# Kernel tuning notes

Measured on AMD Instinct MI355X. Metric: run time of the kernel, lower is better.

The kernel has to match this reference:

```python
import jax, jax.numpy as jnp
import numpy as np

B, T = 2, 2048
D, H = 1024, 16
HD = D // H  # 64
L = 4
V = 32000
DFF = 4 * D
STD = 0.02


def layernorm(x, w, b, eps=1e-5):
    m = jnp.mean(x, axis=-1, keepdims=True)
    v = jnp.var(x, axis=-1, keepdims=True)
    return (x - m) / jnp.sqrt(v + eps) * w + b


def rope(x, cos, sin):
    # x: [B,H,T,HD]; cos/sin: [T, HD//2]
    xe = x[..., ::2]
    xo = x[..., 1::2]
    c = cos[None, None]
    s = sin[None, None]
    re = xe * c - xo * s
    ro = xe * s + xo * c
    return jnp.stack([re, ro], axis=-1).reshape(x.shape)


def setup_inputs() -> dict:
    key = jax.random.key(0)
    ks = jax.random.split(key, 16)
    n = lambda k, shp: jax.random.normal(k, shp, dtype=jnp.float32) * STD
    return {
        "idx": jax.random.randint(ks[0], (B, T), 0, V),
        "tok_emb": n(ks[1], (V, D)),
        "ln1_w": jnp.ones((L, D), jnp.float32),
        "ln1_b": jnp.zeros((L, D), jnp.float32),
        "Wq": n(ks[2], (L, D, D)),
        "Wk": n(ks[3], (L, D, D)),
        "Wv": n(ks[4], (L, D, D)),
        "Wp": n(ks[5], (L, D, D)),
        "ln2_w": jnp.ones((L, D), jnp.float32),
        "ln2_b": jnp.zeros((L, D), jnp.float32),
        "W1": n(ks[6], (L, D, DFF)),
        "b1": jnp.zeros((L, DFF), jnp.float32),
        "W2": n(ks[7], (L, DFF, D)),
        "b2": jnp.zeros((L, D), jnp.float32),
        "lnf_w": jnp.ones((D,), jnp.float32),
        "lnf_b": jnp.zeros((D,), jnp.float32),
    }


def reference(idx, tok_emb, ln1_w, ln1_b, Wq, Wk, Wv, Wp, ln2_w, ln2_b, W1, b1, W2, b2, lnf_w, lnf_b):
    x = tok_emb[idx]  # [B,T,D]
    # RoPE tables (base_freq=10000, no NTK since T == max_seq_len)
    freqs = 1.0 / (10000.0 ** (jnp.arange(0, HD, 2, dtype=jnp.float32) / HD))
    ang = jnp.arange(T, dtype=jnp.float32)[:, None] * freqs[None, :]  # [T, HD/2]
    cos, sin = jnp.cos(ang), jnp.sin(ang)
    causal = jnp.tril(jnp.ones((T, T), dtype=bool))

    def block(x, p):
        l1w, l1b, wq, wk, wv, wp, l2w, l2b, w1, bb1, w2, bb2 = p
        h = layernorm(x, l1w, l1b)
        q = (h @ wq).reshape(B, T, H, HD).transpose(0, 2, 1, 3)
        k = (h @ wk).reshape(B, T, H, HD).transpose(0, 2, 1, 3)
        v = (h @ wv).reshape(B, T, H, HD).transpose(0, 2, 1, 3)
        q = rope(q, cos, sin)
        k = rope(k, cos, sin)
        att = jnp.einsum('bhqd,bhkd->bhqk', q, k) / np.sqrt(HD).astype(np.float32)
        att = jnp.where(causal, att, -jnp.inf)
        att = jax.nn.softmax(att, axis=-1)
        y = jnp.einsum('bhqk,bhkd->bhqd', att, v)
        y = y.transpose(0, 2, 1, 3).reshape(B, T, D)
        x = x + y @ wp
        h2 = layernorm(x, l2w, l2b)
        # torch nn.GELU default = exact erf gelu
        x = x + (jax.nn.gelu(h2 @ w1 + bb1, approximate=False) @ w2 + bb2)
        return x, None

    params = (ln1_w, ln1_b, Wq, Wk, Wv, Wp, ln2_w, ln2_b, W1, b1, W2, b2)
    x, _ = jax.lax.scan(block, x, params)
    x = layernorm(x, lnf_w, lnf_b)
    logits = x @ tok_emb.T  # tied weights
    return logits
```

## Files before the change

kernel.cpp:

```cpp
#include <hip/hip_runtime.h>

#define Bv 2
#define Tv 2048
#define Dv 1024
#define Hv 16
#define HDv 64
#define Lv 4
#define Vv 32000
#define DFFv 4096
#define BTv (Bv * Tv)
#define D3v 3072

typedef __attribute__((ext_vector_type(8))) short bfrag_t;
typedef __attribute__((ext_vector_type(4))) float f4_t;

__device__ __forceinline__ unsigned short f2bf(float f) {
  union { float f; unsigned int u; } cv; cv.f = f;
  unsigned int u = cv.u;
  u += 0x7fffu + ((u >> 16) & 1u);
  return (unsigned short)(u >> 16);
}

__device__ __forceinline__ void gload16(const void* g, void* l) {
  __builtin_amdgcn_global_load_lds((__attribute__((address_space(1))) void*)g,
                                   (__attribute__((address_space(3))) void*)l, 16, 0, 0);
}

__global__ __launch_bounds__(256) void k_cvt(const float* __restrict__ src,
                                             unsigned short* __restrict__ dst, int n4) {
  int i = blockIdx.x * 256 + threadIdx.x;
  if (i >= n4) return;
  float4 v = ((const float4*)src)[i];
  ushort4 o;
  o.x = f2bf(v.x); o.y = f2bf(v.y); o.z = f2bf(v.z); o.w = f2bf(v.w);
  ((ushort4*)dst)[i] = o;
}

__global__ __launch_bounds__(256) void k_embed(const int* __restrict__ idx,
                                               const float* __restrict__ emb,
                                               float* __restrict__ x) {
  int row = blockIdx.x;
  ((float4*)(x + (size_t)row * Dv))[threadIdx.x] =
      ((const float4*)(emb + (size_t)idx[row] * Dv))[threadIdx.x];
}

__global__ __launch_bounds__(256) void k_tcvt(const float* __restrict__ src,
                                              unsigned short* __restrict__ dst,
                                              int R, int C) {
  __shared__ float tile[32][33];
  int c0 = blockIdx.x * 32, r0 = blockIdx.y * 32;
  int tx = threadIdx.x & 31, ty = threadIdx.x >> 5;
#pragma unroll
  for (int i = 0; i < 32; i += 8)
    tile[ty + i][tx] = src[(size_t)(r0 + ty + i) * C + c0 + tx];
  __syncthreads();
#pragma unroll
  for (int i = 0; i < 32; i += 8)
    dst[(size_t)(c0 + ty + i) * R + r0 + tx] = f2bf(tile[tx][ty + i]);
}

__global__ __launch_bounds__(256) void k_ln(const float* __restrict__ x,
                                            const float* __restrict__ w,
                                            const float* __restrict__ b,
                                            unsigned short* __restrict__ out) {
  int row = blockIdx.x, tid = threadIdx.x;
  float4 v = ((const float4*)(x + (size_t)row * Dv))[tid];
  float s = v.x + v.y + v.z + v.w;
  float s2 = v.x * v.x + v.y * v.y + v.z * v.z + v.w * v.w;
#pragma unroll
  for (int off = 32; off > 0; off >>= 1) {
    s += __shfl_xor(s, off);
    s2 += __shfl_xor(s2, off);
  }
  __shared__ float rs[4], rq[4];
  int wv_ = tid >> 6;
  if ((tid & 63) == 0) { rs[wv_] = s; rq[wv_] = s2; }
  __syncthreads();
  s = rs[0] + rs[1] + rs[2] + rs[3];
  s2 = rq[0] + rq[1] + rq[2] + rq[3];
  float mean = s * (1.0f / Dv);
  float var = s2 * (1.0f / Dv) - mean * mean;
  float rstd = rsqrtf(var + 1e-5f);
  float4 wv4 = ((const float4*)w)[tid];
  float4 bv4 = ((const float4*)b)[tid];
  ushort4 o;
  o.x = f2bf((v.x - mean) * rstd * wv4.x + bv4.x);
  o.y = f2bf((v.y - mean) * rstd * wv4.y + bv4.y);
  o.z = f2bf((v.z - mean) * rstd * wv4.z + bv4.z);
  o.w = f2bf((v.w - mean) * rstd * wv4.w + bv4.w);
  ((ushort4*)(out + (size_t)row * Dv))[tid] = o;
}

__global__ __launch_bounds__(256) void k_rope_cvt(const float* __restrict__ qkv,
                                                  unsigned short* __restrict__ qo,
                                                  unsigned short* __restrict__ ko) {
  int g = blockIdx.x * 256 + threadIdx.x;
  int row = g >> 9;
  int p = g & 511;
  int t = row & (Tv - 1);
  int hi = p & 31;
  float freq = (float)exp((double)hi * -0.28782313662425572);
  float ang = (float)t * freq;
  float sn, cs;
  sincosf(ang, &sn, &cs);
  size_t ibase = (size_t)row * D3v + (size_t)(p >> 5) * HDv + (size_t)hi * 2;
  size_t obase = (size_t)row * Dv + (size_t)(p >> 5) * HDv + (size_t)hi * 2;
  float e = qkv[ibase], o = qkv[ibase + 1];
  qo[obase] = f2bf((e * cs - o * sn) * 0.125f);
  qo[obase + 1] = f2bf((e * sn + o * cs) * 0.125f);
  e = qkv[ibase + Dv]; o = qkv[ibase + Dv + 1];
  ko[obase] = f2bf(e * cs - o * sn);
  ko[obase + 1] = f2bf(e * sn + o * cs);
}

__global__ __launch_bounds__(256) void k_vcvt(const float* __restrict__ qkv,
                                              unsigned short* __restrict__ vo) {
  int i = blockIdx.x * 256 + threadIdx.x;
  int row = i >> 8, c4 = (i & 255) * 4;
  float4 v = *(const float4*)(qkv + (size_t)row * D3v + 2 * Dv + c4);
  ushort4 o;
  o.x = f2bf(v.x); o.y = f2bf(v.y); o.z = f2bf(v.z); o.w = f2bf(v.w);
  *(ushort4*)(vo + (size_t)row * Dv + c4) = o;
}

#define AST 72
__global__ __launch_bounds__(256) void k_attn(const unsigned short* __restrict__ q,
                                              const unsigned short* __restrict__ k,
                                              const unsigned short* __restrict__ v,
                                              unsigned short* __restrict__ y) {
  int qt = blockIdx.x, h = blockIdx.y, b = blockIdx.z;
  __shared__ unsigned short Ks[64 * AST];
  __shared__ unsigned short Vt[64 * AST];
  __shared__ unsigned short Ps[64 * AST];
  int tid = threadIdx.x;
  int lane = tid & 63, wave = tid >> 6;
  int lrow = lane & 15, lq = lane >> 4;

  size_t qbase = ((size_t)(b * Tv + qt * 64 + wave * 16 + lrow)) * Dv + h * HDv + lq * 8;
  bfrag_t aq0 = *(const bfrag_t*)(q + qbase);
  bfrag_t aq1 = *(const bfrag_t*)(q + qbase + 32);

  f4_t zero = {0.f, 0.f, 0.f, 0.f};
  f4_t o[4] = {zero, zero, zero, zero};
  float m[4] = {-1e30f, -1e30f, -1e30f, -1e30f};
  float l[4] = {0.f, 0.f, 0.f, 0.f};

  for (int kt = 0; kt <= qt; ++kt) {
    __syncthreads();
    size_t kvbase = ((size_t)(b * Tv + kt * 64)) * Dv + h * HDv;
#pragma unroll
    for (int it = 0; it < 2; ++it) {
      int id = tid + 256 * it;
      int key = id >> 3, d8 = (id & 7) * 8;
      *(bfrag_t*)&Ks[key * AST + d8] =
          *(const bfrag_t*)(k + kvbase + (size_t)key * Dv + d8);
      bfrag_t vv = *(const bfrag_t*)(v + kvbase + (size_t)key * Dv + d8);
#pragma unroll
      for (int j = 0; j < 8; ++j) Vt[(d8 + j) * AST + key] = (unsigned short)vv[j];
    }
    __syncthreads();

    f4_t sacc[4] = {zero, zero, zero, zero};
#pragma unroll
    for (int j = 0; j < 4; ++j) {
      bfrag_t kf0 = *(const bfrag_t*)&Ks[(j * 16 + lrow) * AST + lq * 8];
      bfrag_t kf1 = *(const bfrag_t*)&Ks[(j * 16 + lrow) * AST + 32 + lq * 8];
      sacc[j] = __builtin_amdgcn_mfma_f32_16x16x32_bf16(aq0, kf0, sacc[j], 0, 0, 0);
      sacc[j] = __builtin_amdgcn_mfma_f32_16x16x32_bf16(aq1, kf1, sacc[j], 0, 0, 0);
    }
    if (kt == qt) {
#pragma unroll
      for (int j = 0; j < 4; ++j)
#pragma unroll
        for (int r = 0; r < 4; ++r)
          if (lrow + 16 * j > wave * 16 + lq * 4 + r) sacc[j][r] = -1e30f;
    }

#pragma unroll
    for (int r = 0; r < 4; ++r) {
      float rmax = fmaxf(fmaxf(sacc[0][r], sacc[1][r]), fmaxf(sacc[2][r], sacc[3][r]));
#pragma unroll
      for (int msk = 1; msk < 16; msk <<= 1) rmax = fmaxf(rmax, __shfl_xor(rmax, msk));
      float mn = fmaxf(m[r], rmax);
      float alpha = expf(m[r] - mn);
      m[r] = mn;
      float psum = 0.f;
#pragma unroll
      for (int j = 0; j < 4; ++j) {
        float pv = expf(sacc[j][r] - mn);
        psum += pv;
        Ps[(wave * 16 + lq * 4 + r) * AST + lrow + 16 * j] = f2bf(pv);
      }
#pragma unroll
      for (int msk = 1; msk < 16; msk <<= 1) psum += __shfl_xor(psum, msk);
      l[r] = l[r] * alpha + psum;
      o[0][r] *= alpha; o[1][r] *= alpha; o[2][r] *= alpha; o[3][r] *= alpha;
    }
    __syncthreads();

    bfrag_t pf0 = *(const bfrag_t*)&Ps[(wave * 16 + lrow) * AST + lq * 8];
    bfrag_t pf1 = *(const bfrag_t*)&Ps[(wave * 16 + lrow) * AST + 32 + lq * 8];
#pragma unroll
    for (int dj = 0; dj < 4; ++dj) {
      bfrag_t vf0 = *(const bfrag_t*)&Vt[(dj * 16 + lrow) * AST + lq * 8];
      bfrag_t vf1 = *(const bfrag_t*)&Vt[(dj * 16 + lrow) * AST + 32 + lq * 8];
      o[dj] = __builtin_amdgcn_mfma_f32_16x16x32_bf16(pf0, vf0, o[dj], 0, 0, 0);
      o[dj] = __builtin_amdgcn_mfma_f32_16x16x32_bf16(pf1, vf1, o[dj], 0, 0, 0);
    }
  }

#pragma unroll
  for (int r = 0; r < 4; ++r) {
    float inv = 1.0f / l[r];
    size_t ybo = ((size_t)(b * Tv + qt * 64 + wave * 16 + lq * 4 + r)) * Dv + h * HDv;
#pragma unroll
    for (int dj = 0; dj < 4; ++dj)
      y[ybo + dj * 16 + lrow] = f2bf(o[dj][r] * inv);
  }
}

template <bool BIAS, bool RES, bool GELU, bool OUTF32, bool OUTBF16>
__global__ __launch_bounds__(256) void k_gemm(const unsigned short* __restrict__ A,
                                              const unsigned short* __restrict__ Bt,
                                              const float* __restrict__ bias,
                                              float* __restrict__ C,
                                              unsigned short* __restrict__ Cb,
                                              int M, int N, int K) {
  __shared__ unsigned short As[128 * 32];
  __shared__ unsigned short Bs[128 * 32];
  int tid = threadIdx.x;
  int lane = tid & 63, wave = tid >> 6;

  int nbx = gridDim.x, nby = gridDim.y;
  int bid = blockIdx.y * nbx + blockIdx.x;
  int nwg = nbx * nby;
  int q8 = nwg >> 3, r8 = nwg & 7;
  int xcd = bid & 7, loc = bid >> 3;
  int swz = (xcd < r8 ? xcd * (q8 + 1) : r8 * (q8 + 1) + (xcd - r8) * q8) + loc;
  int panel = 8 * nby;
  int pid = swz / panel;
  int rem = swz - pid * panel;
  int pw = nbx - pid * 8; if (pw > 8) pw = 8;
  int mt = rem / pw;
  int nt = pid * 8 + rem - mt * pw;
  int n0 = nt * 128, m0 = mt * 128;

  int wm = (wave >> 1) * 64, wn = (wave & 1) * 64;
  int lrow = lane & 15, lq = lane >> 4;
  f4_t zero = {0.f, 0.f, 0.f, 0.f};
  f4_t acc[4][4];
#pragma unroll
  for (int i = 0; i < 4; ++i)
#pragma unroll
    for (int j = 0; j < 4; ++j) acc[i][j] = zero;

  int srow_l = lane >> 2;
  int sc = (lane & 3) * 8;
  for (int kk = 0; kk < K; kk += 32) {
#pragma unroll
    for (int it = 0; it < 2; ++it) {
      int seg = wave + 4 * it;
      int srow = seg * 16 + srow_l;
      gload16(A + (size_t)(m0 + srow) * K + kk + sc, &As[seg * 512]);
      gload16(Bt + (size_t)(n0 + srow) * K + kk + sc, &Bs[seg * 512]);
    }
    __syncthreads();
    bfrag_t af[4], bfv[4];
#pragma unroll
    for (int i = 0; i < 4; ++i) {
      af[i] = *(const bfrag_t*)(As + (wm + i * 16 + lrow) * 32 + lq * 8);
      bfv[i] = *(const bfrag_t*)(Bs + (wn + i * 16 + lrow) * 32 + lq * 8);
    }
#pragma unroll
    for (int i = 0; i < 4; ++i)
#pragma unroll
      for (int j = 0; j < 4; ++j)
        acc[i][j] = __builtin_amdgcn_mfma_f32_16x16x32_bf16(af[i], bfv[j], acc[i][j], 0, 0, 0);
    __syncthreads();
  }
#pragma unroll
  for (int i = 0; i < 4; ++i) {
#pragma unroll
    for (int j = 0; j < 4; ++j) {
      int gc = n0 + wn + j * 16 + lrow;
      float bv = BIAS ? bias[gc] : 0.0f;
#pragma unroll
      for (int r = 0; r < 4; ++r) {
        int gr = m0 + wm + i * 16 + lq * 4 + r;
        float val = acc[i][j][r] + bv;
        if (GELU) val = 0.5f * val * (1.0f + erff(val * 0.70710678118654752f));
        size_t ci = (size_t)gr * N + gc;
        if (RES) val += C[ci];
        if (OUTF32) C[ci] = val;
        if (OUTBF16) Cb[ci] = f2bf(val);
      }
    }
  }
}

extern "C" void kernel_launch(void* const* d_in, const int* in_sizes, int n_in,
                              void* d_out, int out_size, void* d_ws, size_t ws_size,
                              hipStream_t stream) {
  const int* idx = (const int*)d_in[0];
  const float* tok = (const float*)d_in[1];
  const float* ln1w = (const float*)d_in[2];
  const float* ln1b = (const float*)d_in[3];
  const float* Wq = (const float*)d_in[4];
  const float* Wk = (const float*)d_in[5];
  const float* Wv = (const float*)d_in[6];
  const float* Wp = (const float*)d_in[7];
  const float* ln2w = (const float*)d_in[8];
  const float* ln2b = (const float*)d_in[9];
  const float* W1 = (const float*)d_in[10];
  const float* b1 = (const float*)d_in[11];
  const float* W2 = (const float*)d_in[12];
  const float* b2 = (const float*)d_in[13];
  const float* lnfw = (const float*)d_in[14];
  const float* lnfb = (const float*)d_in[15];
  float* out = (float*)d_out;

  char* ws = (char*)d_ws;
  size_t off = 0;
  auto alloc = [&](size_t bytes) -> void* {
    void* p = ws + off;
    off += (bytes + 255) & ~(size_t)255;
    return p;
  };
  float* x = (float*)alloc((size_t)BTv * Dv * 4);
  unsigned short* hb = (unsigned short*)alloc((size_t)BTv * Dv * 2);
  float* qkvb = (float*)alloc((size_t)BTv * D3v * 4);
  unsigned short* yb = (unsigned short*)alloc((size_t)BTv * Dv * 2);
  unsigned short* ub = (unsigned short*)alloc((size_t)BTv * DFFv * 2);
  unsigned short* wqkvt = (unsigned short*)alloc((size_t)D3v * Dv * 2);
  unsigned short* wpt = (unsigned short*)alloc((size_t)Dv * Dv * 2);
  unsigned short* w1t = (unsigned short*)alloc((size_t)DFFv * Dv * 2);
  unsigned short* w2t = (unsigned short*)alloc((size_t)Dv * DFFv * 2);
  unsigned short* embb = (unsigned short*)alloc((size_t)Vv * Dv * 2);
  unsigned short* qb16 = ub;
  unsigned short* kb16 = ub + (size_t)BTv * Dv;
  unsigned short* vb16 = ub + (size_t)2 * BTv * Dv;

  k_cvt<<<(Vv * Dv / 4 + 255) / 256, 256, 0, stream>>>(tok, embb, Vv * Dv / 4);
  k_embed<<<BTv, 256, 0, stream>>>(idx, tok, x);
  for (int l = 0; l < Lv; ++l) {
    k_tcvt<<<dim3(Dv / 32, Dv / 32), 256, 0, stream>>>(Wq + (size_t)l * Dv * Dv,
                                                       wqkvt, Dv, Dv);
    k_tcvt<<<dim3(Dv / 32, Dv / 32), 256, 0, stream>>>(Wk + (size_t)l * Dv * Dv,
                                                       wqkvt + (size_t)Dv * Dv, Dv, Dv);
    k_tcvt<<<dim3(Dv / 32, Dv / 32), 256, 0, stream>>>(Wv + (size_t)l * Dv * Dv,
                                                       wqkvt + (size_t)2 * Dv * Dv, Dv, Dv);
    k_tcvt<<<dim3(Dv / 32, Dv / 32), 256, 0, stream>>>(Wp + (size_t)l * Dv * Dv, wpt, Dv, Dv);
    k_tcvt<<<dim3(DFFv / 32, Dv / 32), 256, 0, stream>>>(W1 + (size_t)l * Dv * DFFv, w1t, Dv, DFFv);
    k_tcvt<<<dim3(Dv / 32, DFFv / 32), 256, 0, stream>>>(W2 + (size_t)l * DFFv * Dv, w2t, DFFv, Dv);
    k_ln<<<BTv, 256, 0, stream>>>(x, ln1w + l * Dv, ln1b + l * Dv, hb);
    k_gemm<false, false, false, true, false><<<dim3(D3v / 128, BTv / 128), 256, 0, stream>>>(
        hb, wqkvt, nullptr, qkvb, nullptr, BTv, D3v, Dv);
    k_rope_cvt<<<(BTv * 512) / 256, 256, 0, stream>>>(qkvb, qb16, kb16);
    k_vcvt<<<BTv, 256, 0, stream>>>(qkvb, vb16);
    k_attn<<<dim3(Tv / 64, Hv, Bv), 256, 0, stream>>>(qb16, kb16, vb16, yb);
    k_gemm<false, true, false, true, false><<<dim3(Dv / 128, BTv / 128), 256, 0, stream>>>(
        yb, wpt, nullptr, x, nullptr, BTv, Dv, Dv);
    k_ln<<<BTv, 256, 0, stream>>>(x, ln2w + l * Dv, ln2b + l * Dv, hb);
    k_gemm<true, false, true, false, true><<<dim3(DFFv / 128, BTv / 128), 256, 0, stream>>>(
        hb, w1t, b1 + l * DFFv, nullptr, ub, BTv, DFFv, Dv);
    k_gemm<true, true, false, true, false><<<dim3(Dv / 128, BTv / 128), 256, 0, stream>>>(
        ub, w2t, b2 + l * Dv, x, nullptr, BTv, Dv, DFFv);
  }
  k_ln<<<BTv, 256, 0, stream>>>(x, lnfw, lnfb, hb);
  k_gemm<false, false, false, true, false><<<dim3(Vv / 128, BTv / 128), 256, 0, stream>>>(
      hb, embb, nullptr, out, nullptr, BTv, Vv, Dv);
  (void)in_sizes; (void)n_in; (void)out_size; (void)ws_size;
}
```

Measured before the change: 2.929 ms.

## Add 256x256-tile 8-wave pipelined GEMM for QKV, FC1 and logits

Adds a new bf16 MFMA GEMM that uses 256x256 output tiles and 512 threads (8 waves). It has a 4-deep LDS ring buffer filled by async global-to-LDS loads, an XCD-aware panel swizzle of block indices, and interleaved stage/compute phases with explicit vmcnt waits and setprio. The QKV projection, the FC1+GELU GEMM and the final vocabulary GEMM now use it. The goal is more operand reuse per tile and overlap of memory loads with MFMA work. The trade-off is fewer blocks for the smaller GEMMs, high register and LDS use per block, and hand-tuned wait counts that are fragile.

```diff
diff --git a/kernel.cpp b/kernel.cpp
--- a/kernel.cpp
+++ b/kernel.cpp
@@ -298,6 +298,136 @@
   }
 }
 
+#define VM4 asm volatile("s_waitcnt vmcnt(4)" ::: "memory");
+#define VM0 asm volatile("s_waitcnt vmcnt(0)" ::: "memory");
+#define VMX
+
+#define STAGE_A2(pj)                                                          \
+  {                                                                           \
+    int col_ = ((pj) >> 1) * 64 + ((pj) & 1) * 32 + (schunk ^ sswz) * 8;      \
+    gload16(A + (size_t)(m0 + srow) * K + col_, &As[(pj) & 3][wave * 512]);   \
+    gload16(A + (size_t)(m0 + 128 + srow) * K + col_,                         \
+            &As[(pj) & 3][4096 + wave * 512]);                                \
+  }
+#define STAGE_B2(pj)                                                          \
+  {                                                                           \
+    int col_ = ((pj) >> 1) * 64 + ((pj) & 1) * 32 + (schunk ^ sswz) * 8;      \
+    gload16(Bt + (size_t)(n0 + srow) * K + col_, &Bs[(pj) & 3][wave * 512]);  \
+    gload16(Bt + (size_t)(n0 + 128 + srow) * K + col_,                        \
+            &Bs[(pj) & 3][4096 + wave * 512]);                                \
+  }
+
+#define PHASE2(t_, mh, ks, STAGE, GUARD)                                        \
+  {                                                                             \
+    const unsigned short* As_ = As[(2 * (t_) + (ks)) & 3];                      \
+    const unsigned short* Bs_ = Bs[(2 * (t_) + (ks)) & 3];                      \
+    bfrag_t af[4], bf[4];                                                       \
+    _Pragma("unroll")                                                           \
+    for (int mi = 0; mi < 4; ++mi) {                                            \
+      int row_ = wr * 128 + (mh)*64 + mi * 16 + lrow;                           \
+      af[mi] = *(const bfrag_t*)&As_[row_ * 32 + (lq ^ ((row_ >> 1) & 3)) * 8]; \
+    }                                                                           \
+    _Pragma("unroll")                                                           \
+    for (int ni = 0; ni < 4; ++ni) {                                            \
+      int row_ = wc * 64 + ni * 16 + lrow;                                      \
+      bf[ni] = *(const bfrag_t*)&Bs_[row_ * 32 + (lq ^ ((row_ >> 1) & 3)) * 8]; \
+    }                                                                           \
+    STAGE                                                                       \
+    __builtin_amdgcn_sched_barrier(0);                                          \
+    GUARD                                                                       \
+    __builtin_amdgcn_s_barrier();                                               \
+    __builtin_amdgcn_sched_barrier(0);                                          \
+    __builtin_amdgcn_s_setprio(1);                                              \
+    _Pragma("unroll")                                                           \
+    for (int mi = 0; mi < 4; ++mi)                                              \
+      _Pragma("unroll")                                                         \
+      for (int ni = 0; ni < 4; ++ni)                                            \
+        acc[(mh)*4 + mi][ni] = __builtin_amdgcn_mfma_f32_16x16x32_bf16(         \
+            af[mi], bf[ni], acc[(mh)*4 + mi][ni], 0, 0, 0);                     \
+    __builtin_amdgcn_s_setprio(0);                                              \
+    __builtin_amdgcn_s_barrier();                                               \
+    __builtin_amdgcn_sched_barrier(0);                                          \
+  }
+
+template <bool BIAS, bool RES, bool GELU, bool OUTF32, bool OUTBF16>
+__global__ __launch_bounds__(512, 2) void k_gemm2(const unsigned short* __restrict__ A,
+                                                  const unsigned short* __restrict__ Bt,
+                                                  const float* __restrict__ bias,
+                                                  float* __restrict__ C,
+                                                  unsigned short* __restrict__ Cb,
+                                                  int M, int N, int K) {
+  __shared__ unsigned short As[4][8192];
+  __shared__ unsigned short Bs[4][8192];
+  int tid = threadIdx.x;
+  int lane = tid & 63, wave = tid >> 6;
+  int wr = wave >> 2, wc = wave & 3;
+  int lrow = lane & 15, lq = lane >> 4;
+
+  int nbx = gridDim.x, nby = gridDim.y;
+  int bid = blockIdx.y * nbx + blockIdx.x;
+  int nwg = nbx * nby;
+  int q8 = nwg >> 3, r8 = nwg & 7;
+  int xcd = bid & 7, loc = bid >> 3;
+  int swz = (xcd < r8 ? xcd * (q8 + 1) : r8 * (q8 + 1) + (xcd - r8) * q8) + loc;
+  int panel = 8 * nby;
+  int pid = swz / panel;
+  int rem = swz - pid * panel;
+  int pw = nbx - pid * 8; if (pw > 8) pw = 8;
+  int mt = rem / pw;
+  int nt_ = pid * 8 + rem - mt * pw;
+  int n0 = nt_ * 256, m0 = mt * 256;
+
+  f4_t acc[8][4];
+#pragma unroll
+  for (int i = 0; i < 8; ++i)
+#pragma unroll
+    for (int j = 0; j < 4; ++j) acc[i][j] = (f4_t){0.f, 0.f, 0.f, 0.f};
+
+  const int NT = K >> 6;
+  int srow = tid >> 2;
+  int schunk = tid & 3;
+  int sswz = (srow >> 1) & 3;
+
+  STAGE_A2(0) STAGE_B2(0) STAGE_A2(1) STAGE_B2(1)
+  __builtin_amdgcn_sched_barrier(0);
+  VM4
+  __builtin_amdgcn_s_barrier();
+  __builtin_amdgcn_sched_barrier(0);
+
+  for (int t = 0; t < NT; ++t) {
+    if (t + 1 < NT) {
+      PHASE2(t, 0, 0, STAGE_A2(2 * t + 2), VMX)
+      PHASE2(t, 1, 0, STAGE_B2(2 * t + 2), VM4)
+      PHASE2(t, 0, 1, STAGE_A2(2 * t + 3), VMX)
+      PHASE2(t, 1, 1, STAGE_B2(2 * t + 3), VM4)
+    } else {
+      PHASE2(t, 0, 0, VMX, VMX)
+      PHASE2(t, 1, 0, VMX, VM0)
+      PHASE2(t, 0, 1, VMX, VMX)
+      PHASE2(t, 1, 1, VMX, VMX)
+    }
+  }
+
+#pragma unroll
+  for (int m = 0; m < 8; ++m) {
+#pragma unroll
+    for (int n = 0; n < 4; ++n) {
+      int gc = n0 + wc * 64 + n * 16 + lrow;
+      float bv = BIAS ? bias[gc] : 0.0f;
+#pragma unroll
+      for (int r = 0; r < 4; ++r) {
+        int gr = m0 + wr * 128 + m * 16 + lq * 4 + r;
+        float val = acc[m][n][r] + bv;
+        if (GELU) val = 0.5f * val * (1.0f + erff(val * 0.70710678118654752f));
+        size_t ci = (size_t)gr * N + gc;
+        if (RES) val += C[ci];
+        if (OUTF32) C[ci] = val;
+        if (OUTBF16) Cb[ci] = f2bf(val);
+      }
+    }
+  }
+}
+
 extern "C" void kernel_launch(void* const* d_in, const int* in_sizes, int n_in,
                               void* d_out, int out_size, void* d_ws, size_t ws_size,
                               hipStream_t stream) {
@@ -353,7 +483,7 @@
     k_tcvt<<<dim3(DFFv / 32, Dv / 32), 256, 0, stream>>>(W1 + (size_t)l * Dv * DFFv, w1t, Dv, DFFv);
     k_tcvt<<<dim3(Dv / 32, DFFv / 32), 256, 0, stream>>>(W2 + (size_t)l * DFFv * Dv, w2t, DFFv, Dv);
     k_ln<<<BTv, 256, 0, stream>>>(x, ln1w + l * Dv, ln1b + l * Dv, hb);
-    k_gemm<false, false, false, true, false><<<dim3(D3v / 128, BTv / 128), 256, 0, stream>>>(
+    k_gemm2<false, false, false, true, false><<<dim3(D3v / 256, BTv / 256), 512, 0, stream>>>(
         hb, wqkvt, nullptr, qkvb, nullptr, BTv, D3v, Dv);
     k_rope_cvt<<<(BTv * 512) / 256, 256, 0, stream>>>(qkvb, qb16, kb16);
     k_vcvt<<<BTv, 256, 0, stream>>>(qkvb, vb16);
@@ -361,13 +491,13 @@
     k_gemm<false, true, false, true, false><<<dim3(Dv / 128, BTv / 128), 256, 0, stream>>>(
         yb, wpt, nullptr, x, nullptr, BTv, Dv, Dv);
     k_ln<<<BTv, 256, 0, stream>>>(x, ln2w + l * Dv, ln2b + l * Dv, hb);
-    k_gemm<true, false, true, false, true><<<dim3(DFFv / 128, BTv / 128), 256, 0, stream>>>(
+    k_gemm2<true, false, true, false, true><<<dim3(DFFv / 256, BTv / 256), 512, 0, stream>>>(
         hb, w1t, b1 + l * DFFv, nullptr, ub, BTv, DFFv, Dv);
     k_gemm<true, true, false, true, false><<<dim3(Dv / 128, BTv / 128), 256, 0, stream>>>(
         ub, w2t, b2 + l * Dv, x, nullptr, BTv, Dv, DFFv);
   }
   k_ln<<<BTv, 256, 0, stream>>>(x, lnfw, lnfb, hb);
-  k_gemm<false, false, false, true, false><<<dim3(Vv / 128, BTv / 128), 256, 0, stream>>>(
+  k_gemm2<false, false, false, true, false><<<dim3(Vv / 256, BTv / 256), 512, 0, stream>>>(
       hb, embb, nullptr, out, nullptr, BTv, Vv, Dv);
   (void)in_sizes; (void)n_in; (void)out_size; (void)ws_size;
 }
```

Result: slower. 4.380 ms (+49.6%).
